# Performance work log

Hardware: AMD Instinct MI355X
Metric: run time of the kernel (lower is better)

Reference implementation:

```python
import jax, jax.numpy as jnp
import numpy as np

WL_W = 8   # weight quantization bits (args.wl_weight)
WL_A = 8   # activation quantization bits (args.wl_activate)
EPS = 1e-5


def _quant_ste(x, bits):
    """Symmetric per-tensor uniform quantization with straight-through estimator,
    emulating NeuroSim's wage-style weight/activation quantization in QConv2d."""
    n = float(2 ** (bits - 1) - 1)
    s = jnp.max(jnp.abs(x)) + 1e-12
    xq = jnp.round(x / s * n) / n * s
    return x + jax.lax.stop_gradient(xq - x)


def _qconv(x, w):
    # quantize input and weight, then 3x3 conv, stride 1, padding 1 (NCHW/OIHW)
    xq = _quant_ste(x, WL_A)
    wq = _quant_ste(w, WL_W)
    return jax.lax.conv_general_dilated(
        xq, wq, window_strides=(1, 1), padding=((1, 1), (1, 1)),
        dimension_numbers=('NCHW', 'OIHW', 'NCHW'))


def _bn(x, gamma, beta):
    # training-mode BatchNorm2d: batch statistics over (N, H, W)
    mean = jnp.mean(x, axis=(0, 2, 3), keepdims=True)
    var = jnp.var(x, axis=(0, 2, 3), keepdims=True)
    xn = (x - mean) * jax.lax.rsqrt(var + EPS)
    return xn * gamma[None, :, None, None] + beta[None, :, None, None]


def setup_inputs() -> dict:
    key = jax.random.key(0)
    ks = jax.random.split(key, 3)
    B, C, H, W = 32, 128, 56, 56
    return {
        'x': jax.random.normal(ks[0], (B, C, H, W), dtype=jnp.float32),
        'w1': jax.random.normal(ks[1], (C, C, 3, 3), dtype=jnp.float32) * 0.05,
        'gamma1': jnp.ones((C,), dtype=jnp.float32),
        'beta1': jnp.zeros((C,), dtype=jnp.float32),
        'w2': jax.random.normal(ks[2], (C, C, 3, 3), dtype=jnp.float32) * 0.05,
        'gamma2': jnp.ones((C,), dtype=jnp.float32),
        'beta2': jnp.zeros((C,), dtype=jnp.float32),
    }


def reference(x, w1, gamma1, beta1, w2, gamma2, beta2):
    identity = x  # no downsample
    out = _qconv(x, w1)
    out = _bn(out, gamma1, beta1)
    out = jax.nn.relu(out)
    out = _qconv(out, w2)
    out = _bn(out, gamma2, beta2)
    out = out + identity
    return jax.nn.relu(out)
```

## Files before the change

kernel.cpp:

```cpp
#include <hip/hip_runtime.h>

#define NB 32
#define C 128
#define H 56
#define W 56
#define HWSZ (H*W)
#define ELTS (NB*C*HWSZ)
#define NHW (NB*HWSZ)
#define HP 59
#define SLAB 8192
#define NBCOL (H*NB)

typedef __attribute__((ext_vector_type(8))) short bf16x8;
typedef __attribute__((ext_vector_type(4))) short short4v;
typedef __attribute__((ext_vector_type(4))) float f32x4;
typedef __attribute__((ext_vector_type(4))) int i32x4;

#define SLOT_SX 0
#define SLOT_SW1 1
#define SLOT_SW2 2
#define SLOT_SA2 3
#define SUM1 8
#define SSQ1 136
#define MAXE1 264
#define MAXNEG1 392
#define SCALE1 520
#define SHIFT1 648
#define SUM2 776
#define SSQ2 904
#define MAXE2 1032
#define MAXNEG2 1160
#define SCALE2 1288
#define SHIFT2 1416

#define META_OFF 0ull
#define META_BYTES 8192ull
#define XQ_OFF 8192ull
#define XQ_BYTES ((unsigned long long)NB*HP*SLAB)
#define A2Q_OFF (XQ_OFF + XQ_BYTES)
#define Y1_OFF (A2Q_OFF + XQ_BYTES)
#define Y_BYTES ((unsigned long long)ELTS*2ull)
#define Y2_OFF (Y1_OFF + Y_BYTES)
#define W1Q_OFF (Y2_OFF + Y_BYTES)
#define WQ_BYTES (9ull*2*128*64)
#define W2Q_OFF (W1Q_OFF + WQ_BYTES)
#define PART_OFF (W2Q_OFF + WQ_BYTES)
#define PART_BYTES ((unsigned long long)NBCOL*512*4)

__device__ __forceinline__ short f2bf_rne(float f) {
    unsigned u = __float_as_uint(f);
    return (short)((u + 0x7FFFu + ((u >> 16) & 1u)) >> 16);
}
__device__ __forceinline__ float bf2f(short s) {
    return __uint_as_float(((unsigned)(unsigned short)s) << 16);
}
__device__ __forceinline__ unsigned fenc(float f) {
    unsigned u = __float_as_uint(f);
    return (u & 0x80000000u) ? ~u : (u | 0x80000000u);
}
__device__ __forceinline__ float fdec(unsigned e) {
    unsigned u = (e & 0x80000000u) ? (e ^ 0x80000000u) : ~e;
    return __uint_as_float(u);
}

__global__ void absmax_kernel(const float* __restrict__ p, int n4, unsigned* __restrict__ slot) {
    __shared__ float red[256];
    float m = 0.f;
    int stride = gridDim.x * blockDim.x;
    for (int i = blockIdx.x * blockDim.x + threadIdx.x; i < n4; i += stride) {
        f32x4 v = ((const f32x4*)p)[i];
        m = fmaxf(m, fmaxf(fmaxf(fabsf(v.x), fabsf(v.y)), fmaxf(fabsf(v.z), fabsf(v.w))));
    }
    red[threadIdx.x] = m;
    __syncthreads();
    for (int s = 128; s > 0; s >>= 1) {
        if (threadIdx.x < s) red[threadIdx.x] = fmaxf(red[threadIdx.x], red[threadIdx.x + s]);
        __syncthreads();
    }
    if (threadIdx.x == 0) atomicMax(slot, __float_as_uint(red[0]));
}

__global__ void absmax_w_kernel(const float* __restrict__ w1, const float* __restrict__ w2,
                                unsigned* __restrict__ metau) {
    __shared__ float red[256];
    const float* p = blockIdx.y ? w2 : w1;
    unsigned* slot = metau + (blockIdx.y ? SLOT_SW2 : SLOT_SW1);
    const int n4 = 147456 / 4;
    float m = 0.f;
    int stride = gridDim.x * blockDim.x;
    for (int i = blockIdx.x * blockDim.x + threadIdx.x; i < n4; i += stride) {
        f32x4 v = ((const f32x4*)p)[i];
        m = fmaxf(m, fmaxf(fmaxf(fabsf(v.x), fabsf(v.y)), fmaxf(fabsf(v.z), fabsf(v.w))));
    }
    red[threadIdx.x] = m;
    __syncthreads();
    for (int s = 128; s > 0; s >>= 1) {
        if (threadIdx.x < s) red[threadIdx.x] = fmaxf(red[threadIdx.x], red[threadIdx.x + s]);
        __syncthreads();
    }
    if (threadIdx.x == 0) atomicMax(slot, __float_as_uint(red[0]));
}

__global__ void pad_zero_kernel(char* __restrict__ xq, char* __restrict__ a2q,
                                float* __restrict__ meta) {
    int hp = blockIdx.x;
    int n = blockIdx.y;
    char* base = (blockIdx.z ? a2q : xq) + ((size_t)n * HP + hp) * SLAB;
    int t = threadIdx.x;
    if (blockIdx.z == 0 && blockIdx.x == 0 && blockIdx.y == 0) {
        #pragma unroll
        for (int j = 0; j < 8; ++j) meta[j * 256 + t] = 0.f;
    }
    if (hp == 0 || hp >= 57) {
        f32x4 z = {0.f, 0.f, 0.f, 0.f};
        *(f32x4*)(base + t * 16) = z;
        *(f32x4*)(base + 4096 + t * 16) = z;
    } else {
        if (t < 32) *(int*)(base + t * 4) = 0;
        else        *(int*)(base + 7296 + (t - 32) * 4) = 0;
    }
}

__global__ void quant_w_kernel(const float* __restrict__ w1, const float* __restrict__ w2,
                               const float* __restrict__ meta,
                               char* __restrict__ w1q, char* __restrict__ w2q) {
    const float* w = blockIdx.y ? w2 : w1;
    char* wq = blockIdx.y ? w2q : w1q;
    float qs = 127.f / (meta[blockIdx.y ? SLOT_SW2 : SLOT_SW1] + 1e-12f);
    int idx = blockIdx.x * 256 + threadIdx.x;
    int co = idx >> 7, ci = idx & 127;
    const float* src = w + ((size_t)(co * 128 + ci)) * 9;
    int cc = ci >> 6, cl = ci & 63;
    #pragma unroll
    for (int tap = 0; tap < 9; ++tap) {
        int q = (int)rintf(src[tap] * qs);
        wq[(((size_t)tap * 2 + cc) * 128 + co) * 64 + cl] = (char)q;
    }
}

__global__ void quant_x_kernel(const float* __restrict__ x, const float* __restrict__ meta,
                               char* __restrict__ xq) {
    __shared__ float tile[128][57];
    int h = blockIdx.x, n = blockIdx.y, t = threadIdx.x;
    int ci = t >> 1, seg = (t & 1) * 28;
    const float* row = x + (((size_t)(n * C + ci)) * H + h) * W + seg;
    #pragma unroll
    for (int j = 0; j < 28; j += 4) {
        f32x4 v = *(const f32x4*)(row + j);
        tile[ci][seg + j + 0] = v.x;
        tile[ci][seg + j + 1] = v.y;
        tile[ci][seg + j + 2] = v.z;
        tile[ci][seg + j + 3] = v.w;
    }
    __syncthreads();
    float qs = 127.f / (meta[SLOT_SX] + 1e-12f);
    int w = t & 63, cq = t >> 6;
    if (w < 56) {
        char* slab = xq + ((size_t)n * HP + (h + 1)) * SLAB;
        int wp = w + 1;
        #pragma unroll
        for (int c2 = 0; c2 < 2; ++c2) {
            union { char c[16]; i32x4 v; } u;
            #pragma unroll
            for (int j = 0; j < 16; ++j)
                u.c[j] = (char)(int)rintf(tile[cq * 32 + c2 * 16 + j][w] * qs);
            int L = wp * 128 + cq * 32 + c2 * 16;
            *(i32x4*)(slab + (L ^ ((wp & 7) << 4))) = u.v;
        }
    }
}

__global__ __launch_bounds__(256, 4) void conv_mfma_kernel(
        const char* __restrict__ xq, const char* __restrict__ wq,
        short* __restrict__ y, const float* __restrict__ meta,
        float* __restrict__ part, int slot_in, int slot_w) {
    __shared__ __align__(16) char lds[3 * SLAB + 512 + 2048];
    const int n = blockIdx.y, h = blockIdx.x;
    const int t = threadIdx.x, lane = t & 63;
    const int co0 = (t >> 6) * 32;
    const int l15 = lane & 15, lg = lane >> 4;

    const char* slabbase = xq + ((size_t)n * HP + h) * SLAB;
    #pragma unroll
    for (int s = 0; s < 3; ++s) {
        #pragma unroll
        for (int i = 0; i < 2; ++i) {
            int off = (i * 256 + t) * 16;
            __builtin_amdgcn_global_load_lds(
                (const __attribute__((address_space(1))) unsigned*)(slabbase + s * SLAB + off),
                (__attribute__((address_space(3))) unsigned*)(lds + s * SLAB + off), 16, 0, 0);
        }
    }

    i32x4 acc[2][4] = {};

    #pragma unroll
    for (int kh = 0; kh < 3; ++kh) {
        if (kh == 0)      { asm volatile("s_waitcnt vmcnt(4)" ::: "memory"); }
        else if (kh == 1) { asm volatile("s_waitcnt vmcnt(2)" ::: "memory"); }
        else              { asm volatile("s_waitcnt vmcnt(0)" ::: "memory"); }
        __builtin_amdgcn_s_barrier();
        const char* Bb = lds + kh * SLAB;
        #pragma unroll
        for (int kw = 0; kw < 3; ++kw) {
            #pragma unroll
            for (int cc = 0; cc < 2; ++cc) {
                const char* wt = wq + (((kh * 3 + kw) * 2 + cc) << 13);
                i32x4 a[2];
                #pragma unroll
                for (int ct = 0; ct < 2; ++ct)
                    a[ct] = *(const i32x4*)(wt + (co0 + ct * 16 + l15) * 64 + lg * 16);
                #pragma unroll
                for (int fj = 0; fj < 4; ++fj) {
                    int wpp = fj * 16 + l15 + kw;
                    int L = (wpp << 7) + (cc << 6) + (lg << 4);
                    i32x4 b = *(const i32x4*)(Bb + (L ^ ((wpp & 7) << 4)));
                    #pragma unroll
                    for (int ct = 0; ct < 2; ++ct)
                        acc[ct][fj] = __builtin_amdgcn_mfma_i32_16x16x64_i8(a[ct], b, acc[ct][fj], 0, 0, 0);
                }
            }
        }
    }

    float dq = (meta[slot_in] + 1e-12f) * (meta[slot_w] + 1e-12f) * (1.f / 16129.f);
    short* yrow = y + (((size_t)n * H + h) * W) * C;
    float* slds = (float*)(lds + 3 * SLAB + 512);

    #pragma unroll
    for (int ct = 0; ct < 2; ++ct) {
        float s1[4] = {}, s2[4] = {}, m1[4], m2[4];
        #pragma unroll
        for (int q = 0; q < 4; ++q) { m1[q] = -1e30f; m2[q] = -1e30f; }
        #pragma unroll
        for (int fj = 0; fj < 4; ++fj) {
            int wo = fj * 16 + l15;
            if (wo < W) {
                short4v pk;
                #pragma unroll
                for (int q = 0; q < 4; ++q) {
                    float v = (float)acc[ct][fj][q] * dq;
                    s1[q] += v;
                    s2[q] += v * v;
                    m1[q] = fmaxf(m1[q], v);
                    m2[q] = fmaxf(m2[q], -v);
                    pk[q] = f2bf_rne(v);
                }
                *(short4v*)(yrow + (size_t)wo * C + co0 + ct * 16 + lg * 4) = pk;
            }
        }
        #pragma unroll
        for (int q = 0; q < 4; ++q) {
            #pragma unroll
            for (int m = 1; m < 16; m <<= 1) {
                s1[q] += __shfl_xor(s1[q], m, 64);
                s2[q] += __shfl_xor(s2[q], m, 64);
                m1[q] = fmaxf(m1[q], __shfl_xor(m1[q], m, 64));
                m2[q] = fmaxf(m2[q], __shfl_xor(m2[q], m, 64));
            }
        }
        if (l15 == 0) {
            #pragma unroll
            for (int q = 0; q < 4; ++q) {
                int c = co0 + ct * 16 + lg * 4 + q;
                slds[0 * 128 + c] = s1[q];
                slds[1 * 128 + c] = s2[q];
                slds[2 * 128 + c] = m1[q];
                slds[3 * 128 + c] = m2[q];
            }
        }
    }
    __syncthreads();
    if (t < 128) {
        int p = t >> 5, cs = (t & 31) * 4;
        f32x4 sv = *(const f32x4*)(slds + p * 128 + cs);
        size_t bcol = (size_t)n * H + h;
        *(f32x4*)(part + bcol * 512 + p * 128 + cs) = sv;
    }
}

__global__ void bn_reduce_kernel(const float* __restrict__ part, float* __restrict__ meta,
                                 int sum_off, int ssq_off, int maxe_off, int maxneg_off) {
    int t = threadIdx.x, b = blockIdx.x;
    const float* base = part + (size_t)b * 28 * 512;
    float vadd = 0.f, vmax = -1e30f;
    for (int i = 0; i < 28; ++i) {
        vadd += base[i * 512 + t];
        vmax = fmaxf(vmax, base[i * 512 + 256 + t]);
    }
    int c = t & 127;
    unsigned* metau = (unsigned*)meta;
    if (t < 128) {
        atomicAdd(&meta[sum_off + c], vadd);
        atomicMax(metau + maxe_off + c, fenc(vmax));
    } else {
        atomicAdd(&meta[ssq_off + c], vadd);
        atomicMax(metau + maxneg_off + c, fenc(vmax));
    }
}

__global__ void bn_finalize_kernel(float* __restrict__ meta, int sum_off, int ssq_off,
                                   int maxe_off, int maxneg_off, int scale_off, int shift_off,
                                   int amax_slot,
                                   const float* __restrict__ gamma, const float* __restrict__ beta) {
    __shared__ float red[128];
    int c = threadIdx.x;
    float mean = meta[sum_off + c] * (1.f / NHW);
    float var = meta[ssq_off + c] * (1.f / NHW) - mean * mean;
    float istd = rsqrtf(var + 1e-5f);
    float sc = gamma[c] * istd;
    float sh = beta[c] - mean * sc;
    meta[scale_off + c] = sc;
    meta[shift_off + c] = sh;
    if (amax_slot >= 0) {
        float vmax = fdec(((unsigned*)meta)[maxe_off + c]);
        float vmin = -fdec(((unsigned*)meta)[maxneg_off + c]);
        float cand = fmaxf(0.f, fmaxf(sc * vmax + sh, sc * vmin + sh));
        red[c] = cand;
        __syncthreads();
        for (int k = 64; k > 0; k >>= 1) {
            if (c < k) red[c] = fmaxf(red[c], red[c + k]);
            __syncthreads();
        }
        if (c == 0) meta[amax_slot] = red[0];
    }
}

__global__ void quant_bnrelu_kernel(const short* __restrict__ y1, const float* __restrict__ meta,
                                    char* __restrict__ a2q) {
    int h = blockIdx.x, n = blockIdx.y, t = threadIdx.x;
    const short* row = y1 + (((size_t)n * H + h) * W) * C;
    float qs = 127.f / (meta[SLOT_SA2] + 1e-12f);
    char* slab = a2q + ((size_t)n * HP + (h + 1)) * SLAB;
    #pragma unroll
    for (int i = 0; i < 2; ++i) {
        int g = i * 256 + t;
        if (g < 448) {
            int w = g >> 3, cg = g & 7;
            bf16x8 v0 = *(const bf16x8*)(row + w * 128 + cg * 16);
            bf16x8 v1 = *(const bf16x8*)(row + w * 128 + cg * 16 + 8);
            union { char c[16]; i32x4 v; } u;
            #pragma unroll
            for (int j = 0; j < 8; ++j) {
                float a = fmaxf(bf2f(v0[j]) * meta[SCALE1 + cg * 16 + j] + meta[SHIFT1 + cg * 16 + j], 0.f);
                u.c[j] = (char)(int)rintf(a * qs);
            }
            #pragma unroll
            for (int j = 0; j < 8; ++j) {
                float a = fmaxf(bf2f(v1[j]) * meta[SCALE1 + cg * 16 + 8 + j] + meta[SHIFT1 + cg * 16 + 8 + j], 0.f);
                u.c[8 + j] = (char)(int)rintf(a * qs);
            }
            int wp = w + 1;
            int L = wp * 128 + cg * 16;
            *(i32x4*)(slab + (L ^ ((wp & 7) << 4))) = u.v;
        }
    }
}

__global__ void final_kernel(const short* __restrict__ y2, const float* __restrict__ x,
                             const float* __restrict__ meta, float* __restrict__ out) {
    __shared__ short tile[56 * 128];
    int h = blockIdx.x, n = blockIdx.y, t = threadIdx.x;
    const short* row = y2 + (((size_t)n * H + h) * W) * C;
    #pragma unroll
    for (int i = 0; i < 4; ++i) {
        int g = i * 256 + t;
        if (g < 896) *(bf16x8*)(tile + g * 8) = *(const bf16x8*)(row + g * 8);
    }
    __syncthreads();
    int c = t >> 1, seg = (t & 1) * 28;
    float sc = meta[SCALE2 + c], sh = meta[SHIFT2 + c];
    const float* xr = x + (((size_t)(n * C + c)) * H + h) * W + seg;
    float* orow = out + (((size_t)(n * C + c)) * H + h) * W + seg;
    #pragma unroll
    for (int j = 0; j < 28; j += 4) {
        f32x4 xv = *(const f32x4*)(xr + j);
        f32x4 o;
        #pragma unroll
        for (int k = 0; k < 4; ++k) {
            float yv = bf2f(tile[(seg + j + k) * 128 + c]);
            o[k] = fmaxf(yv * sc + sh + xv[k], 0.f);
        }
        *(f32x4*)(orow + j) = o;
    }
}

extern "C" void kernel_launch(void* const* d_in, const int* in_sizes, int n_in,
                              void* d_out, int out_size, void* d_ws, size_t ws_size,
                              hipStream_t stream) {
    const float* x      = (const float*)d_in[0];
    const float* w1     = (const float*)d_in[1];
    const float* gamma1 = (const float*)d_in[2];
    const float* beta1  = (const float*)d_in[3];
    const float* w2     = (const float*)d_in[4];
    const float* gamma2 = (const float*)d_in[5];
    const float* beta2  = (const float*)d_in[6];
    float* out = (float*)d_out;
    char* ws = (char*)d_ws;

    float* meta = (float*)(ws + META_OFF);
    unsigned* metau = (unsigned*)meta;
    char* xq   = ws + XQ_OFF;
    char* a2q  = ws + A2Q_OFF;
    short* y1  = (short*)(ws + Y1_OFF);
    short* y2  = (short*)(ws + Y2_OFF);
    char* w1q  = ws + W1Q_OFF;
    char* w2q  = ws + W2Q_OFF;
    float* part = (float*)(ws + PART_OFF);

    pad_zero_kernel<<<dim3(59, 32, 2), 256, 0, stream>>>(xq, a2q, meta);

    absmax_kernel<<<1024, 256, 0, stream>>>(x, ELTS / 4, metau + SLOT_SX);
    absmax_w_kernel<<<dim3(64, 2), 256, 0, stream>>>(w1, w2, metau);
    quant_w_kernel<<<dim3(64, 2), 256, 0, stream>>>(w1, w2, meta, w1q, w2q);

    dim3 ghn(56, 32);
    quant_x_kernel<<<ghn, 256, 0, stream>>>(x, meta, xq);

    conv_mfma_kernel<<<ghn, 256, 0, stream>>>(xq, w1q, y1, meta, part, SLOT_SX, SLOT_SW1);
    bn_reduce_kernel<<<64, 256, 0, stream>>>(part, meta, SUM1, SSQ1, MAXE1, MAXNEG1);
    bn_finalize_kernel<<<1, 128, 0, stream>>>(meta, SUM1, SSQ1, MAXE1, MAXNEG1,
                                              SCALE1, SHIFT1, SLOT_SA2, gamma1, beta1);
    quant_bnrelu_kernel<<<ghn, 256, 0, stream>>>(y1, meta, a2q);

    conv_mfma_kernel<<<ghn, 256, 0, stream>>>(a2q, w2q, y2, meta, part, SLOT_SA2, SLOT_SW2);
    bn_reduce_kernel<<<64, 256, 0, stream>>>(part, meta, SUM2, SSQ2, MAXE2, MAXNEG2);
    bn_finalize_kernel<<<1, 128, 0, stream>>>(meta, SUM2, SSQ2, MAXE2, MAXNEG2,
                                              SCALE2, SHIFT2, -1, gamma2, beta2);

    final_kernel<<<ghn, 256, 0, stream>>>(y2, x, meta, out);
}
```

Before: 251.5 us.

## Merge absmax/quant launches and fold BN finalize into reduce via last-block counter

Combines the activation and weight absmax kernels into one launch, folds weight quantization into the activation quantization kernel as extra blocks, and removes the separate BN finalize kernels by having the last finishing reduce block (tracked with an atomic counter) compute scale/shift. It also replaces the staged vmcnt waits in the conv kernel with a single __syncthreads after all LDS loads. This cuts four kernel launches and their gaps, but the conv change gives up overlap between the tap-row loads and MFMA compute, and the last-block pattern adds atomics and a threadfence.

```diff
diff --git a/kernel.cpp b/kernel.cpp
--- a/kernel.cpp
+++ b/kernel.cpp
@@ -20,6 +20,8 @@
 #define SLOT_SW1 1
 #define SLOT_SW2 2
 #define SLOT_SA2 3
+#define CNT1 4
+#define CNT2 5
 #define SUM1 8
 #define SSQ1 136
 #define MAXE1 264
@@ -63,32 +65,19 @@
     return __uint_as_float(u);
 }
 
-__global__ void absmax_kernel(const float* __restrict__ p, int n4, unsigned* __restrict__ slot) {
+__global__ void absmax_all_kernel(const float* __restrict__ x, const float* __restrict__ w1,
+                                  const float* __restrict__ w2, unsigned* __restrict__ metau) {
     __shared__ float red[256];
+    const float* p;
+    unsigned* slot;
+    int n4, b0, nb;
+    int b = blockIdx.x;
+    if (b < 1024)      { p = x;  slot = metau + SLOT_SX;  n4 = ELTS / 4;   b0 = b;        nb = 1024; }
+    else if (b < 1088) { p = w1; slot = metau + SLOT_SW1; n4 = 147456 / 4; b0 = b - 1024; nb = 64; }
+    else               { p = w2; slot = metau + SLOT_SW2; n4 = 147456 / 4; b0 = b - 1088; nb = 64; }
     float m = 0.f;
-    int stride = gridDim.x * blockDim.x;
-    for (int i = blockIdx.x * blockDim.x + threadIdx.x; i < n4; i += stride) {
-        f32x4 v = ((const f32x4*)p)[i];
-        m = fmaxf(m, fmaxf(fmaxf(fabsf(v.x), fabsf(v.y)), fmaxf(fabsf(v.z), fabsf(v.w))));
-    }
-    red[threadIdx.x] = m;
-    __syncthreads();
-    for (int s = 128; s > 0; s >>= 1) {
-        if (threadIdx.x < s) red[threadIdx.x] = fmaxf(red[threadIdx.x], red[threadIdx.x + s]);
-        __syncthreads();
-    }
-    if (threadIdx.x == 0) atomicMax(slot, __float_as_uint(red[0]));
-}
-
-__global__ void absmax_w_kernel(const float* __restrict__ w1, const float* __restrict__ w2,
-                                unsigned* __restrict__ metau) {
-    __shared__ float red[256];
-    const float* p = blockIdx.y ? w2 : w1;
-    unsigned* slot = metau + (blockIdx.y ? SLOT_SW2 : SLOT_SW1);
-    const int n4 = 147456 / 4;
-    float m = 0.f;
-    int stride = gridDim.x * blockDim.x;
-    for (int i = blockIdx.x * blockDim.x + threadIdx.x; i < n4; i += stride) {
+    int stride = nb * 256;
+    for (int i = b0 * 256 + threadIdx.x; i < n4; i += stride) {
         f32x4 v = ((const f32x4*)p)[i];
         m = fmaxf(m, fmaxf(fmaxf(fabsf(v.x), fabsf(v.y)), fmaxf(fabsf(v.z), fabsf(v.w))));
     }
@@ -121,27 +110,29 @@
     }
 }
 
-__global__ void quant_w_kernel(const float* __restrict__ w1, const float* __restrict__ w2,
-                               const float* __restrict__ meta,
-                               char* __restrict__ w1q, char* __restrict__ w2q) {
-    const float* w = blockIdx.y ? w2 : w1;
-    char* wq = blockIdx.y ? w2q : w1q;
-    float qs = 127.f / (meta[blockIdx.y ? SLOT_SW2 : SLOT_SW1] + 1e-12f);
-    int idx = blockIdx.x * 256 + threadIdx.x;
-    int co = idx >> 7, ci = idx & 127;
-    const float* src = w + ((size_t)(co * 128 + ci)) * 9;
-    int cc = ci >> 6, cl = ci & 63;
-    #pragma unroll
-    for (int tap = 0; tap < 9; ++tap) {
-        int q = (int)rintf(src[tap] * qs);
-        wq[(((size_t)tap * 2 + cc) * 128 + co) * 64 + cl] = (char)q;
-    }
-}
-
-__global__ void quant_x_kernel(const float* __restrict__ x, const float* __restrict__ meta,
-                               char* __restrict__ xq) {
+__global__ void quant_xw_kernel(const float* __restrict__ x,
+                                const float* __restrict__ w1, const float* __restrict__ w2,
+                                const float* __restrict__ meta, char* __restrict__ xq,
+                                char* __restrict__ w1q, char* __restrict__ w2q) {
     __shared__ float tile[128][57];
-    int h = blockIdx.x, n = blockIdx.y, t = threadIdx.x;
+    int bx = blockIdx.x, n = blockIdx.y, t = threadIdx.x;
+    if (bx >= 56) {
+        int wid = (bx - 56) * 32 + n;
+        const float* w = (wid >= 64) ? w2 : w1;
+        char* wq = (wid >= 64) ? w2q : w1q;
+        float qs = 127.f / (meta[(wid >= 64) ? SLOT_SW2 : SLOT_SW1] + 1e-12f);
+        int idx = (wid & 63) * 256 + t;
+        int co = idx >> 7, ci = idx & 127;
+        const float* src = w + ((size_t)(co * 128 + ci)) * 9;
+        int cc = ci >> 6, cl = ci & 63;
+        #pragma unroll
+        for (int tap = 0; tap < 9; ++tap) {
+            int q = (int)rintf(src[tap] * qs);
+            wq[(((size_t)tap * 2 + cc) * 128 + co) * 64 + cl] = (char)q;
+        }
+        return;
+    }
+    int h = bx;
     int ci = t >> 1, seg = (t & 1) * 28;
     const float* row = x + (((size_t)(n * C + ci)) * H + h) * W + seg;
     #pragma unroll
@@ -191,15 +182,12 @@
                 (__attribute__((address_space(3))) unsigned*)(lds + s * SLAB + off), 16, 0, 0);
         }
     }
+    __syncthreads();
 
     i32x4 acc[2][4] = {};
 
     #pragma unroll
     for (int kh = 0; kh < 3; ++kh) {
-        if (kh == 0)      { asm volatile("s_waitcnt vmcnt(4)" ::: "memory"); }
-        else if (kh == 1) { asm volatile("s_waitcnt vmcnt(2)" ::: "memory"); }
-        else              { asm volatile("s_waitcnt vmcnt(0)" ::: "memory"); }
-        __builtin_amdgcn_s_barrier();
         const char* Bb = lds + kh * SLAB;
         #pragma unroll
         for (int kw = 0; kw < 3; ++kw) {
@@ -280,7 +268,9 @@
 }
 
 __global__ void bn_reduce_kernel(const float* __restrict__ part, float* __restrict__ meta,
-                                 int sum_off, int ssq_off, int maxe_off, int maxneg_off) {
+                                 const float* __restrict__ gamma, const float* __restrict__ beta,
+                                 int sum_off, int ssq_off, int maxe_off, int maxneg_off,
+                                 int scale_off, int shift_off, int amax_slot, int counter_off) {
     int t = threadIdx.x, b = blockIdx.x;
     const float* base = part + (size_t)b * 28 * 512;
     float vadd = 0.f, vmax = -1e30f;
@@ -297,32 +287,33 @@
         atomicAdd(&meta[ssq_off + c], vadd);
         atomicMax(metau + maxneg_off + c, fenc(vmax));
     }
-}
-
-__global__ void bn_finalize_kernel(float* __restrict__ meta, int sum_off, int ssq_off,
-                                   int maxe_off, int maxneg_off, int scale_off, int shift_off,
-                                   int amax_slot,
-                                   const float* __restrict__ gamma, const float* __restrict__ beta) {
+    __threadfence();
+    __shared__ unsigned lastdone;
     __shared__ float red[128];
-    int c = threadIdx.x;
-    float mean = meta[sum_off + c] * (1.f / NHW);
-    float var = meta[ssq_off + c] * (1.f / NHW) - mean * mean;
-    float istd = rsqrtf(var + 1e-5f);
-    float sc = gamma[c] * istd;
-    float sh = beta[c] - mean * sc;
-    meta[scale_off + c] = sc;
-    meta[shift_off + c] = sh;
+    if (t == 0) lastdone = atomicAdd(metau + counter_off, 1u);
+    __syncthreads();
+    if (lastdone != 63) return;
+    if (t < 128) {
+        float sum = atomicAdd(&meta[sum_off + c], 0.f);
+        float ssq = atomicAdd(&meta[ssq_off + c], 0.f);
+        float vmx = fdec(atomicMax(metau + maxe_off + c, 0u));
+        float vmn = -fdec(atomicMax(metau + maxneg_off + c, 0u));
+        float mean = sum * (1.f / NHW);
+        float var = ssq * (1.f / NHW) - mean * mean;
+        float istd = rsqrtf(var + 1e-5f);
+        float sc = gamma[c] * istd;
+        float sh = beta[c] - mean * sc;
+        meta[scale_off + c] = sc;
+        meta[shift_off + c] = sh;
+        red[c] = fmaxf(0.f, fmaxf(sc * vmx + sh, sc * vmn + sh));
+    }
+    __syncthreads();
     if (amax_slot >= 0) {
-        float vmax = fdec(((unsigned*)meta)[maxe_off + c]);
-        float vmin = -fdec(((unsigned*)meta)[maxneg_off + c]);
-        float cand = fmaxf(0.f, fmaxf(sc * vmax + sh, sc * vmin + sh));
-        red[c] = cand;
-        __syncthreads();
         for (int k = 64; k > 0; k >>= 1) {
-            if (c < k) red[c] = fmaxf(red[c], red[c + k]);
+            if (t < k) red[t] = fmaxf(red[t], red[t + k]);
             __syncthreads();
         }
-        if (c == 0) meta[amax_slot] = red[0];
+        if (t == 0) meta[amax_slot] = red[0];
     }
 }
 
@@ -409,24 +400,21 @@
     float* part = (float*)(ws + PART_OFF);
 
     pad_zero_kernel<<<dim3(59, 32, 2), 256, 0, stream>>>(xq, a2q, meta);
-
-    absmax_kernel<<<1024, 256, 0, stream>>>(x, ELTS / 4, metau + SLOT_SX);
-    absmax_w_kernel<<<dim3(64, 2), 256, 0, stream>>>(w1, w2, metau);
-    quant_w_kernel<<<dim3(64, 2), 256, 0, stream>>>(w1, w2, meta, w1q, w2q);
+    absmax_all_kernel<<<1152, 256, 0, stream>>>(x, w1, w2, metau);
 
     dim3 ghn(56, 32);
-    quant_x_kernel<<<ghn, 256, 0, stream>>>(x, meta, xq);
+    quant_xw_kernel<<<dim3(60, 32), 256, 0, stream>>>(x, w1, w2, meta, xq, w1q, w2q);
 
     conv_mfma_kernel<<<ghn, 256, 0, stream>>>(xq, w1q, y1, meta, part, SLOT_SX, SLOT_SW1);
-    bn_reduce_kernel<<<64, 256, 0, stream>>>(part, meta, SUM1, SSQ1, MAXE1, MAXNEG1);
-    bn_finalize_kernel<<<1, 128, 0, stream>>>(meta, SUM1, SSQ1, MAXE1, MAXNEG1,
-                                              SCALE1, SHIFT1, SLOT_SA2, gamma1, beta1);
+    bn_reduce_kernel<<<64, 256, 0, stream>>>(part, meta, gamma1, beta1,
+                                             SUM1, SSQ1, MAXE1, MAXNEG1,
+                                             SCALE1, SHIFT1, SLOT_SA2, CNT1);
     quant_bnrelu_kernel<<<ghn, 256, 0, stream>>>(y1, meta, a2q);
 
     conv_mfma_kernel<<<ghn, 256, 0, stream>>>(a2q, w2q, y2, meta, part, SLOT_SA2, SLOT_SW2);
-    bn_reduce_kernel<<<64, 256, 0, stream>>>(part, meta, SUM2, SSQ2, MAXE2, MAXNEG2);
-    bn_finalize_kernel<<<1, 128, 0, stream>>>(meta, SUM2, SSQ2, MAXE2, MAXNEG2,
-                                              SCALE2, SHIFT2, -1, gamma2, beta2);
+    bn_reduce_kernel<<<64, 256, 0, stream>>>(part, meta, gamma2, beta2,
+                                             SUM2, SSQ2, MAXE2, MAXNEG2,
+                                             SCALE2, SHIFT2, -1, CNT2);
 
     final_kernel<<<ghn, 256, 0, stream>>>(y2, x, meta, out);
 }
```

Measured after the change: 252.6 us. About the same (+0.4%).
